# Performance work log

Hardware: AMD Instinct MI355X
Metric: run time of the kernel (lower is better)

## Reference

```python
import jax, jax.numpy as jnp
import numpy as np

B, S, E = 8, 1024, 1024
MS = 128            # modal_context seq len
NH = 16             # attention heads
NE = 8              # total experts (4 shared + 4 modality-specific)
TOP_K = 2
FF = 4 * E          # expert hidden dim
EPS = 1e-5


def layer_norm(x, w, b, eps=EPS):
    m = jnp.mean(x, axis=-1, keepdims=True)
    v = jnp.mean(jnp.square(x - m), axis=-1, keepdims=True)
    return (x - m) / jnp.sqrt(v + eps) * w + b


def mha(q_in, kv_in, in_w, in_b, out_w, out_b, nh=NH):
    # torch nn.MultiheadAttention (batch_first) equivalent, eval mode (no dropout)
    e = q_in.shape[-1]
    q = q_in @ in_w[:e].T + in_b[:e]
    k = kv_in @ in_w[e:2 * e].T + in_b[e:2 * e]
    v = kv_in @ in_w[2 * e:].T + in_b[2 * e:]
    b, sq, _ = q.shape
    sk = k.shape[1]
    hd = e // nh
    q = q.reshape(b, sq, nh, hd).transpose(0, 2, 1, 3)
    k = k.reshape(b, sk, nh, hd).transpose(0, 2, 1, 3)
    v = v.reshape(b, sk, nh, hd).transpose(0, 2, 1, 3)
    scores = jnp.einsum('bhqd,bhkd->bhqk', q, k) * (1.0 / np.sqrt(hd).astype(np.float32))
    attn = jax.nn.softmax(scores, axis=-1)
    o = jnp.einsum('bhqk,bhkd->bhqd', attn, v).transpose(0, 2, 1, 3).reshape(b, sq, e)
    return o @ out_w.T + out_b


def _forward(x, modal_context,
             attn_in_w, attn_in_b, attn_out_w, attn_out_b,
             xattn_in_w, xattn_in_b, xattn_out_w, xattn_out_b,
             norm1_w, norm1_b, norm2_w, norm2_b, norm3_w, norm3_b,
             xnorm_w, xnorm_b, router_w, router_b, gate_w, gate_b,
             exp_ln_w, exp_ln_b, exp_fc1_w, exp_fc1_b, exp_fc2_w, exp_fc2_b):
    # --- self-attention block (pre-norm residual) ---
    h = x + mha(layer_norm(x, norm1_w, norm1_b), layer_norm(x, norm1_w, norm1_b),
                attn_in_w, attn_in_b, attn_out_w, attn_out_b)
    # --- cross-modal fusion with sigmoid modal gate ---
    xn = layer_norm(h, xnorm_w, xnorm_b)
    fusion = mha(xn, modal_context, xattn_in_w, xattn_in_b, xattn_out_w, xattn_out_b)
    gate = jax.nn.sigmoid(xn @ gate_w.T + gate_b)
    h = h + gate * fusion
    # --- MoE block: AttentiveRouter (softmax + top-k renorm) over shared+modality experts ---
    xn2 = layer_norm(h, norm2_w, norm2_b)
    logits = xn2 @ router_w.T + router_b                  # [B,S,NE]
    probs = jax.nn.softmax(logits, axis=-1)
    topw, topi = jax.lax.top_k(probs, TOP_K)              # [B,S,K]
    topw = topw / jnp.sum(topw, axis=-1, keepdims=True)
    # scatter top-k weights to dense combine tensor [B,S,NE]
    combine = jnp.sum(jax.nn.one_hot(topi, NE, dtype=x.dtype) * topw[..., None], axis=-2)
    moe = jnp.zeros_like(h)
    for e_idx in range(NE):  # small fixed loop over experts
        xe = layer_norm(xn2, exp_ln_w[e_idx], exp_ln_b[e_idx])
        hh = jax.nn.gelu(xe @ exp_fc1_w[e_idx].T + exp_fc1_b[e_idx])
        oe = hh @ exp_fc2_w[e_idx].T + exp_fc2_b[e_idx]
        moe = moe + combine[..., e_idx:e_idx + 1] * oe
    out = h + moe
    return layer_norm(out, norm3_w, norm3_b)


def setup_inputs() -> dict:
    key = jax.random.key(0)
    ks = jax.random.split(key, 32)
    std = 0.02
    d = {
        'x': jax.random.normal(ks[0], (B, S, E), jnp.float32),
        'modal_context': jax.random.normal(ks[1], (B, MS, E), jnp.float32),
        'attn_in_w': jax.random.normal(ks[2], (3 * E, E), jnp.float32) * std,
        'attn_in_b': jnp.zeros((3 * E,), jnp.float32),
        'attn_out_w': jax.random.normal(ks[3], (E, E), jnp.float32) * std,
        'attn_out_b': jnp.zeros((E,), jnp.float32),
        'xattn_in_w': jax.random.normal(ks[4], (3 * E, E), jnp.float32) * std,
        'xattn_in_b': jnp.zeros((3 * E,), jnp.float32),
        'xattn_out_w': jax.random.normal(ks[5], (E, E), jnp.float32) * std,
        'xattn_out_b': jnp.zeros((E,), jnp.float32),
        'norm1_w': jnp.ones((E,), jnp.float32), 'norm1_b': jnp.zeros((E,), jnp.float32),
        'norm2_w': jnp.ones((E,), jnp.float32), 'norm2_b': jnp.zeros((E,), jnp.float32),
        'norm3_w': jnp.ones((E,), jnp.float32), 'norm3_b': jnp.zeros((E,), jnp.float32),
        'xnorm_w': jnp.ones((E,), jnp.float32), 'xnorm_b': jnp.zeros((E,), jnp.float32),
        'router_w': jax.random.normal(ks[6], (NE, E), jnp.float32) * 0.1 / np.sqrt(E).astype(np.float32),
        'router_b': jnp.zeros((NE,), jnp.float32),
        'gate_w': jax.random.normal(ks[7], (E, E), jnp.float32) * std,
        'gate_b': jnp.zeros((E,), jnp.float32),
        'exp_ln_w': jnp.ones((NE, E), jnp.float32),
        'exp_ln_b': jnp.zeros((NE, E), jnp.float32),
        'exp_fc1_w': jax.random.normal(ks[8], (NE, FF, E), jnp.float32) * std,
        'exp_fc1_b': jnp.zeros((NE, FF), jnp.float32),
        'exp_fc2_w': jax.random.normal(ks[9], (NE, E, FF), jnp.float32) * std,
        'exp_fc2_b': jnp.zeros((NE, E), jnp.float32),
    }
    return d


def reference(x, modal_context,
              attn_in_w, attn_in_b, attn_out_w, attn_out_b,
              xattn_in_w, xattn_in_b, xattn_out_w, xattn_out_b,
              norm1_w, norm1_b, norm2_w, norm2_b, norm3_w, norm3_b,
              xnorm_w, xnorm_b, router_w, router_b, gate_w, gate_b,
              exp_ln_w, exp_ln_b, exp_fc1_w, exp_fc1_b, exp_fc2_w, exp_fc2_b):
    return _forward(x, modal_context,
                    attn_in_w, attn_in_b, attn_out_w, attn_out_b,
                    xattn_in_w, xattn_in_b, xattn_out_w, xattn_out_b,
                    norm1_w, norm1_b, norm2_w, norm2_b, norm3_w, norm3_b,
                    xnorm_w, xnorm_b, router_w, router_b, gate_w, gate_b,
                    exp_ln_w, exp_ln_b, exp_fc1_w, exp_fc1_b, exp_fc2_w, exp_fc2_b)
```

## Files before the change

### kernel.cpp

```cpp
#include <hip/hip_runtime.h>
#include <cstdint>
#include <cstddef>
#include <math.h>

typedef unsigned short u16;
typedef __attribute__((ext_vector_type(4))) float f32x4;
typedef __attribute__((ext_vector_type(8))) short short8;
typedef __attribute__((ext_vector_type(4))) short short4v;

__device__ __forceinline__ float b2f(u16 u) {
    union { unsigned int i; float f; } v; v.i = ((unsigned int)u) << 16; return v.f;
}
__device__ __forceinline__ u16 f2b(float f) {
    union { float f; unsigned int i; } v; v.f = f;
    unsigned int i = v.i;
    return (u16)((i + 0x7FFFu + ((i >> 16) & 1u)) >> 16);
}
__device__ __forceinline__ void split3t(float a, short& h, short& m, short& l) {
    union { float f; unsigned int u; } va, vh, v1, vm, v2;
    va.f = a;
    vh.u = va.u & 0xFFFF0000u;
    float r1 = a - vh.f;
    v1.f = r1;
    vm.u = v1.u & 0xFFFF0000u;
    float r2 = r1 - vm.f;
    v2.f = r2;
    h = (short)(vh.u >> 16);
    m = (short)(vm.u >> 16);
    l = (short)(v2.u >> 16);
}
__device__ __forceinline__ float gelu_f(float x) {
    float x3 = x * x * x;
    float y = 0.7978845608028654f * (x + 0.044715f * x3);
    float ya = fminf(fabsf(y), 15.f);
    float e = expf(-2.f * ya);
    float t = (1.f - e) / (1.f + e);
    t = copysignf(t, y);
    return 0.5f * x * (1.f + t);
}
__device__ __forceinline__ void gld16(const u16* g, u16* l)
{
    __builtin_amdgcn_global_load_lds(
        (const __attribute__((address_space(1))) void*)(g),
        (__attribute__((address_space(3))) void*)(l),
        16, 0, 0);
}

struct EGemmP {
    const float* A; int lda; long aSo, aSi; int aDiv;
    const float* B; int ldb; long bSo, bSi; int bDiv;
    float* C; int ldc; long cSo, cSi; int cDiv;
    const float* bias;
    const float* resid;
    const float* fus;
    int K;
};

template<int EPI, int WM, int WN, int MF, int NF>
__global__ __launch_bounds__(256)
void gemm_emu(EGemmP p)
{
    constexpr int TM = WM * MF * 16;
    constexpr int TN = WN * NF * 16;
    constexpr int TK = 32;
    __shared__ u16 Ah[TM * TK], Am[TM * TK], Al[TM * TK];
    __shared__ u16 Bh[TN * TK], Bm[TN * TK], Bl[TN * TK];
    const int tid = threadIdx.x;
    const int z = blockIdx.z;
    const float* Ab = p.A + (long)(z / p.aDiv) * p.aSo + (long)(z % p.aDiv) * p.aSi
                      + (long)blockIdx.x * TM * p.lda;
    const float* Bb = p.B + (long)(z / p.bDiv) * p.bSo + (long)(z % p.bDiv) * p.bSi
                      + (long)blockIdx.y * TN * p.ldb;
    const int lane = tid & 63;
    const int wv = tid >> 6;
    const int wm = wv / WN;
    const int wn = wv % WN;
    const int kg = lane >> 4;
    const int l16 = lane & 15;
    f32x4 acc[MF][NF];
#pragma unroll
    for (int m = 0; m < MF; ++m)
#pragma unroll
        for (int n = 0; n < NF; ++n)
            acc[m][n] = (f32x4){0.f, 0.f, 0.f, 0.f};

    for (int k0 = 0; k0 < p.K; k0 += TK) {
#pragma unroll
        for (int i = 0; i < (TM * TK) / 1024; ++i) {
            int e = i * 256 + tid;
            int r = e >> 3;
            int c = (e & 7) * 4;
            f32x4 a = *(const f32x4*)&Ab[(long)r * p.lda + k0 + c];
            short4v h, m, l;
#pragma unroll
            for (int j = 0; j < 4; ++j) {
                short th, tm2, tl2;
                split3t(a[j], th, tm2, tl2);
                h[j] = th; m[j] = tm2; l[j] = tl2;
            }
            *(short4v*)&Ah[r * TK + c] = h;
            *(short4v*)&Am[r * TK + c] = m;
            *(short4v*)&Al[r * TK + c] = l;
        }
#pragma unroll
        for (int i = 0; i < (TN * TK) / 1024; ++i) {
            int e = i * 256 + tid;
            int r = e >> 3;
            int c = (e & 7) * 4;
            f32x4 a = *(const f32x4*)&Bb[(long)r * p.ldb + k0 + c];
            short4v h, m, l;
#pragma unroll
            for (int j = 0; j < 4; ++j) {
                short th, tm2, tl2;
                split3t(a[j], th, tm2, tl2);
                h[j] = th; m[j] = tm2; l[j] = tl2;
            }
            *(short4v*)&Bh[r * TK + c] = h;
            *(short4v*)&Bm[r * TK + c] = m;
            *(short4v*)&Bl[r * TK + c] = l;
        }
        __syncthreads();
        short8 ah[MF], am[MF], al[MF], bh[NF], bm[NF], bl[NF];
#pragma unroll
        for (int m = 0; m < MF; ++m) {
            int ro = (wm * MF * 16 + m * 16 + l16) * TK + kg * 8;
            ah[m] = *(const short8*)&Ah[ro];
            am[m] = *(const short8*)&Am[ro];
            al[m] = *(const short8*)&Al[ro];
        }
#pragma unroll
        for (int n = 0; n < NF; ++n) {
            int ro = (wn * NF * 16 + n * 16 + l16) * TK + kg * 8;
            bh[n] = *(const short8*)&Bh[ro];
            bm[n] = *(const short8*)&Bm[ro];
            bl[n] = *(const short8*)&Bl[ro];
        }
#pragma unroll
        for (int m = 0; m < MF; ++m)
#pragma unroll
            for (int n = 0; n < NF; ++n) {
                f32x4 a = acc[m][n];
                a = __builtin_amdgcn_mfma_f32_16x16x32_bf16(al[m], bh[n], a, 0, 0, 0);
                a = __builtin_amdgcn_mfma_f32_16x16x32_bf16(ah[m], bl[n], a, 0, 0, 0);
                a = __builtin_amdgcn_mfma_f32_16x16x32_bf16(am[m], bm[n], a, 0, 0, 0);
                a = __builtin_amdgcn_mfma_f32_16x16x32_bf16(am[m], bh[n], a, 0, 0, 0);
                a = __builtin_amdgcn_mfma_f32_16x16x32_bf16(ah[m], bm[n], a, 0, 0, 0);
                a = __builtin_amdgcn_mfma_f32_16x16x32_bf16(ah[m], bh[n], a, 0, 0, 0);
                acc[m][n] = a;
            }
        __syncthreads();
    }
    const long cbase = (long)(z / p.cDiv) * p.cSo + (long)(z % p.cDiv) * p.cSi;
#pragma unroll
    for (int m = 0; m < MF; ++m)
#pragma unroll
        for (int n = 0; n < NF; ++n) {
            const int colt = blockIdx.y * TN + wn * NF * 16 + n * 16 + l16;
            float bv = p.bias ? p.bias[colt] : 0.f;
#pragma unroll
            for (int r = 0; r < 4; ++r) {
                const int rowt = blockIdx.x * TM + wm * MF * 16 + m * 16 + kg * 4 + r;
                const long idx = cbase + (long)rowt * p.ldc + colt;
                float v = acc[m][n][r] + bv;
                if constexpr (EPI == 0) {
                    p.C[idx] = v;
                } else if constexpr (EPI == 1) {
                    p.C[idx] = v + p.resid[idx];
                } else {
                    float g = 1.f / (1.f + expf(-v));
                    p.C[idx] = p.resid[idx] + g * p.fus[idx];
                }
            }
        }
}

struct MoeP {
    const u16* A; int lda;
    const u16* Bw; long bStrideE; int ldb;
    u16* HHo;
    float* M1; float* M2;
    int ldc;
    const float* biasE; long biasStride;
    const float* combine;
    const int* cnt;
    const int* pfx;
    const int* tlist;
    int K;
};

template<int EPI>
__global__ __launch_bounds__(256)
void gemm_moe(MoeP p)
{
    const int ex = blockIdx.z;
    const int count = p.cnt[ex];
    if ((int)(blockIdx.x * 128) >= count) return;
    const int base = p.pfx[ex];
    constexpr int TK = 64;
    __shared__ __align__(16) u16 lA[128 * TK];
    __shared__ __align__(16) u16 lB[128 * TK];
    const int tid = threadIdx.x;
    const u16* Ab = p.A + (long)(base + blockIdx.x * 128) * p.lda;
    const u16* Bb = p.Bw + (long)ex * p.bStrideE + (long)blockIdx.y * 128 * p.ldb;
    const int lane = tid & 63;
    const int wv = tid >> 6;
    const int wm = wv >> 1;
    const int wn = wv & 1;
    const int kg = lane >> 4;
    const int l16 = lane & 15;
    f32x4 acc[4][4];
#pragma unroll
    for (int m = 0; m < 4; ++m)
#pragma unroll
        for (int n = 0; n < 4; ++n)
            acc[m][n] = (f32x4){0.f, 0.f, 0.f, 0.f};

    const u16* pa[4]; const u16* pb[4]; u16* la[4]; u16* lb[4];
#pragma unroll
    for (int i = 0; i < 4; ++i) {
        int e = i * 256 + tid;
        int r = e >> 3;
        int jg = (e & 7) ^ (r & 7);
        pa[i] = &Ab[(long)r * p.lda + jg * 8];
        pb[i] = &Bb[(long)r * p.ldb + jg * 8];
        la[i] = &lA[e * 8];
        lb[i] = &lB[e * 8];
    }

    for (int k0 = 0; k0 < p.K; k0 += TK) {
#pragma unroll
        for (int i = 0; i < 4; ++i) {
            gld16(pa[i] + k0, la[i]);
            gld16(pb[i] + k0, lb[i]);
        }
        __syncthreads();
#pragma unroll
        for (int ks = 0; ks < 2; ++ks) {
            short8 af[4], bfr[4];
#pragma unroll
            for (int m = 0; m < 4; ++m) {
                int row = wm * 64 + m * 16 + l16;
                int jj = (ks * 4 + kg) ^ (row & 7);
                af[m] = *(const short8*)&lA[row * TK + jj * 8];
            }
#pragma unroll
            for (int n = 0; n < 4; ++n) {
                int row = wn * 64 + n * 16 + l16;
                int jj = (ks * 4 + kg) ^ (row & 7);
                bfr[n] = *(const short8*)&lB[row * TK + jj * 8];
            }
#pragma unroll
            for (int m = 0; m < 4; ++m)
#pragma unroll
                for (int n = 0; n < 4; ++n)
                    acc[m][n] = __builtin_amdgcn_mfma_f32_16x16x32_bf16(af[m], bfr[n], acc[m][n], 0, 0, 0);
        }
        __syncthreads();
    }
    const float* bias = p.biasE + (long)ex * p.biasStride;
#pragma unroll
    for (int m = 0; m < 4; ++m)
#pragma unroll
        for (int n = 0; n < 4; ++n) {
            const int colt = blockIdx.y * 128 + wn * 64 + n * 16 + l16;
            const float bv = bias[colt];
#pragma unroll
            for (int r = 0; r < 4; ++r) {
                const int rowt = blockIdx.x * 128 + wm * 64 + m * 16 + kg * 4 + r;
                if (rowt >= count) continue;
                float v = acc[m][n][r] + bv;
                if constexpr (EPI == 3) {
                    p.HHo[(long)(base + rowt) * p.ldc + colt] = f2b(gelu_f(v));
                } else {
                    const int entry = p.tlist[ex * 8192 + rowt];
                    const int tok = entry & 0xFFFF;
                    const int k = entry >> 16;
                    const float w = p.combine[(long)tok * 8 + ex];
                    float* dst = k ? p.M2 : p.M1;
                    dst[(long)tok * p.ldc + colt] = w * v;
                }
            }
        }
}

template<int MODE>
__global__ __launch_bounds__(256)
void ln2p(const float* in, const float* add1, const float* add2,
          const float* w, const float* b, float* outf)
{
    const long row = blockIdx.x;
    const int t = threadIdx.x;
    const int c0 = t * 4;
    f32x4 v = *(const f32x4*)&in[row * 1024 + c0];
    if constexpr (MODE == 2) {
        f32x4 a1 = *(const f32x4*)&add1[row * 1024 + c0];
        f32x4 a2 = *(const f32x4*)&add2[row * 1024 + c0];
#pragma unroll
        for (int j = 0; j < 4; ++j) v[j] += a1[j] + a2[j];
    }
    __shared__ float r1[4], r2[4];
    const int lane = t & 63, wv = t >> 6;
    float s1 = v[0] + v[1] + v[2] + v[3];
    for (int o = 32; o; o >>= 1) s1 += __shfl_xor(s1, o);
    if (lane == 0) r1[wv] = s1;
    __syncthreads();
    const float mean = (r1[0] + r1[1] + r1[2] + r1[3]) * (1.f / 1024.f);
    f32x4 d;
#pragma unroll
    for (int j = 0; j < 4; ++j) d[j] = v[j] - mean;
    float s2 = d[0] * d[0] + d[1] * d[1] + d[2] * d[2] + d[3] * d[3];
    for (int o = 32; o; o >>= 1) s2 += __shfl_xor(s2, o);
    if (lane == 0) r2[wv] = s2;
    __syncthreads();
    const float var = (r2[0] + r2[1] + r2[2] + r2[3]) * (1.f / 1024.f);
    const float rstd = 1.f / sqrtf(var + 1e-5f);
    f32x4 o4;
#pragma unroll
    for (int j = 0; j < 4; ++j) o4[j] = d[j] * rstd * w[c0 + j] + b[c0 + j];
    *(f32x4*)&outf[row * 1024 + c0] = o4;
}

__global__ __launch_bounds__(256)
void rowstats(const float* in, float* st, int* cnt)
{
    if (blockIdx.x == 0 && threadIdx.x < 8) cnt[threadIdx.x] = 0;
    const long row = blockIdx.x;
    const int t = threadIdx.x;
    const int c0 = t * 4;
    f32x4 v = *(const f32x4*)&in[row * 1024 + c0];
    __shared__ float r1[4], r2[4];
    const int lane = t & 63, wv = t >> 6;
    float s1 = v[0] + v[1] + v[2] + v[3];
    for (int o = 32; o; o >>= 1) s1 += __shfl_xor(s1, o);
    if (lane == 0) r1[wv] = s1;
    __syncthreads();
    const float mean = (r1[0] + r1[1] + r1[2] + r1[3]) * (1.f / 1024.f);
    float s2 = 0.f;
#pragma unroll
    for (int j = 0; j < 4; ++j) { float d = v[j] - mean; s2 += d * d; }
    for (int o = 32; o; o >>= 1) s2 += __shfl_xor(s2, o);
    if (lane == 0) r2[wv] = s2;
    __syncthreads();
    if (t == 0) {
        const float var = (r2[0] + r2[1] + r2[2] + r2[3]) * (1.f / 1024.f);
        st[row * 2] = mean;
        st[row * 2 + 1] = 1.f / sqrtf(var + 1e-5f);
    }
}

__global__ __launch_bounds__(256)
void softmax_f32(float* sm, int C, float scale)
{
    const long row = blockIdx.x;
    float* p = sm + row * (long)C;
    const int t = threadIdx.x;
    const int idx = t * 4;
    const bool act = idx < C;
    f32x4 v = (f32x4){-1e30f, -1e30f, -1e30f, -1e30f};
    if (act) {
        v = *(const f32x4*)&p[idx];
#pragma unroll
        for (int j = 0; j < 4; ++j) v[j] *= scale;
    }
    float mx = fmaxf(fmaxf(v[0], v[1]), fmaxf(v[2], v[3]));
    for (int o = 32; o; o >>= 1) mx = fmaxf(mx, __shfl_xor(mx, o));
    __shared__ float red[4], red2[4];
    const int lane = t & 63, wv = t >> 6;
    if (lane == 0) red[wv] = mx;
    __syncthreads();
    mx = fmaxf(fmaxf(red[0], red[1]), fmaxf(red[2], red[3]));
    float e[4], s = 0.f;
    if (act) {
#pragma unroll
        for (int j = 0; j < 4; ++j) { e[j] = expf(v[j] - mx); s += e[j]; }
    }
    for (int o = 32; o; o >>= 1) s += __shfl_xor(s, o);
    if (lane == 0) red2[wv] = s;
    __syncthreads();
    s = red2[0] + red2[1] + red2[2] + red2[3];
    if (act) {
        f32x4 o4;
#pragma unroll
        for (int j = 0; j < 4; ++j) o4[j] = e[j] / s;
        *(f32x4*)&p[idx] = o4;
    }
}

__global__ __launch_bounds__(256)
void transpose64f(const float* src, int sld, long sSo, long sSi, int sDiv, float* dst, int Skv)
{
    const int z = blockIdx.y;
    const float* Sp = src + (long)(z / sDiv) * sSo + (long)(z % sDiv) * sSi;
    float* Dp = dst + (long)z * 64 * Skv;
    const int j0 = blockIdx.x * 64;
    __shared__ float tl[64][68];
    const int tid = threadIdx.x;
#pragma unroll
    for (int it = 0; it < 4; ++it) {
        int e = (it * 256 + tid) * 4;
        int r = e >> 6, c = e & 63;
        f32x4 d = *(const f32x4*)&Sp[(long)(j0 + r) * sld + c];
        *(f32x4*)&tl[r][c] = d;
    }
    __syncthreads();
    const int d0 = tid >> 2;
    const int jc = (tid & 3) * 16;
    float tmp[16];
#pragma unroll
    for (int i = 0; i < 16; ++i) tmp[i] = tl[jc + i][d0];
#pragma unroll
    for (int i = 0; i < 16; ++i) Dp[(long)d0 * Skv + j0 + jc + i] = tmp[i];
}

__global__ __launch_bounds__(256)
void router_k(const float* xn2, const float* rw, const float* rb, float* cmb,
              int* cnt, int* tlist)
{
    const int tok = blockIdx.x * 4 + (threadIdx.x >> 6);
    const int lane = threadIdx.x & 63;
    const float* xp = xn2 + (long)tok * 1024 + lane * 16;
    float xv[16];
#pragma unroll
    for (int j = 0; j < 16; ++j) xv[j] = xp[j];
    double acc[8];
#pragma unroll
    for (int e = 0; e < 8; ++e) {
        const float* wp = rw + e * 1024 + lane * 16;
        double s = 0.0;
#pragma unroll
        for (int j = 0; j < 16; ++j) s += (double)xv[j] * (double)wp[j];
        acc[e] = s;
    }
    for (int o = 32; o; o >>= 1) {
#pragma unroll
        for (int e = 0; e < 8; ++e) acc[e] += __shfl_xor(acc[e], o);
    }
    if (lane == 0) {
        double l[8];
#pragma unroll
        for (int e = 0; e < 8; ++e) l[e] = acc[e] + (double)rb[e];
        int i1 = 0;
#pragma unroll
        for (int e = 1; e < 8; ++e) if (l[e] > l[i1]) i1 = e;
        int i2 = (i1 == 0) ? 1 : 0;
#pragma unroll
        for (int e = 0; e < 8; ++e) if (e != i1 && l[e] > l[i2]) i2 = e;
        double w1 = 1.0 / (1.0 + exp(l[i2] - l[i1]));
        double w2 = 1.0 - w1;
        float c8[8] = {0, 0, 0, 0, 0, 0, 0, 0};
        c8[i1] = (float)w1;
        c8[i2] = (float)w2;
        float* cp = cmb + (long)tok * 8;
#pragma unroll
        for (int e = 0; e < 8; ++e) cp[e] = c8[e];
        int s1 = atomicAdd(&cnt[i1], 1);
        tlist[i1 * 8192 + s1] = tok;
        int s2 = atomicAdd(&cnt[i2], 1);
        tlist[i2 * 8192 + s2] = tok | 65536;
    }
}

__global__ void prefix8(const int* cnt, int* pfx)
{
    if (threadIdx.x == 0) {
        int s = 0;
#pragma unroll
        for (int e = 0; e < 8; ++e) { pfx[e] = s; s += cnt[e]; }
    }
}

__global__ __launch_bounds__(256)
void gather_all(const float* xn2, const float* st, const int* cnt, const int* pfx,
                const int* tlist, const float* lnw, const float* lnb, u16* xe)
{
    const int e = blockIdx.y;
    const int slot = blockIdx.x;
    if (slot >= cnt[e]) return;
    const int tok = tlist[e * 8192 + slot] & 0xFFFF;
    const int c0 = threadIdx.x * 4;
    f32x4 v = *(const f32x4*)&xn2[(long)tok * 1024 + c0];
    const float m = st[tok * 2], r = st[tok * 2 + 1];
    const float* w = lnw + (long)e * 1024;
    const float* b = lnb + (long)e * 1024;
    short4v o4;
#pragma unroll
    for (int j = 0; j < 4; ++j) o4[j] = (short)f2b((v[j] - m) * r * w[c0 + j] + b[c0 + j]);
    *(short4v*)&xe[(long)(pfx[e] + slot) * 1024 + c0] = o4;
}

__global__ __launch_bounds__(256)
void cvtw(const float* in, u16* out, long n4)
{
    const long stride = (long)gridDim.x * 256;
    for (long i = (long)blockIdx.x * 256 + threadIdx.x; i < n4; i += stride) {
        f32x4 v = *(const f32x4*)&in[i * 4];
        short4v o;
#pragma unroll
        for (int j = 0; j < 4; ++j) o[j] = (short)f2b(v[j]);
        *(short4v*)&out[i * 4] = o;
    }
}

extern "C" void kernel_launch(void* const* d_in, const int* in_sizes, int n_in,
                              void* d_out, int out_size, void* d_ws, size_t ws_size,
                              hipStream_t stream)
{
    (void)in_sizes; (void)n_in; (void)out_size;
    const float* x          = (const float*)d_in[0];
    const float* modal      = (const float*)d_in[1];
    const float* attn_in_w  = (const float*)d_in[2];
    const float* attn_in_b  = (const float*)d_in[3];
    const float* attn_out_w = (const float*)d_in[4];
    const float* attn_out_b = (const float*)d_in[5];
    const float* xattn_in_w = (const float*)d_in[6];
    const float* xattn_in_b = (const float*)d_in[7];
    const float* xattn_out_w= (const float*)d_in[8];
    const float* xattn_out_b= (const float*)d_in[9];
    const float* norm1_w = (const float*)d_in[10];
    const float* norm1_b = (const float*)d_in[11];
    const float* norm2_w = (const float*)d_in[12];
    const float* norm2_b = (const float*)d_in[13];
    const float* norm3_w = (const float*)d_in[14];
    const float* norm3_b = (const float*)d_in[15];
    const float* xnorm_w = (const float*)d_in[16];
    const float* xnorm_b = (const float*)d_in[17];
    const float* router_w = (const float*)d_in[18];
    const float* router_b = (const float*)d_in[19];
    const float* gate_w = (const float*)d_in[20];
    const float* gate_b = (const float*)d_in[21];
    const float* exp_ln_w = (const float*)d_in[22];
    const float* exp_ln_b = (const float*)d_in[23];
    const float* exp_fc1_w = (const float*)d_in[24];
    const float* exp_fc1_b = (const float*)d_in[25];
    const float* exp_fc2_w = (const float*)d_in[26];
    const float* exp_fc2_b = (const float*)d_in[27];

    char* wsb = (char*)d_ws;
    size_t off = 0;
    auto AL = [&](size_t bytes) { size_t r = off; off += (bytes + 255) & ~(size_t)255; return r; };
    float* XN  = (float*)(wsb + AL(33554432));
    float* H   = (float*)(wsb + AL(33554432));
    float* H2  = (float*)(wsb + AL(33554432));
    float* XN2 = (float*)(wsb + AL(33554432));
    float* FUS = (float*)(wsb + AL(33554432));
    float* MOE = (float*)(wsb + AL(33554432));
    float* XKV = (float*)(wsb + AL(8388608));
    float* CMB = (float*)(wsb + AL(262144));
    float* ST  = (float*)(wsb + AL(65536));
    int*   CNT = (int*)(wsb + AL(256));
    int*   PFX = (int*)(wsb + AL(256));
    int*   TLS = (int*)(wsb + AL(262144));
    char*  RA  = wsb + AL(100663296);
    char*  RB  = wsb + AL(100663296);
    if (off > ws_size) return;

    float* QKV = (float*)RA;
    float* XQ  = (float*)RA;
    float* XO  = (float*)(RA + 33554432);
    float* SCf = (float*)RB;
    float* VTf = (float*)(RB + 67108864);
    float* SC2 = H2;
    u16*   HH  = (u16*)RA;
    u16*   XE  = (u16*)(RA + 135266304);
    u16*   WB  = (u16*)XN;
    float* out = (float*)d_out;

    ln2p<0><<<8192, 256, 0, stream>>>(x, nullptr, nullptr, norm1_w, norm1_b, XN);

    {
        EGemmP p{XN, 1024, 0, 0, 1, attn_in_w, 1024, 0, 0, 1,
                 QKV, 3072, 0, 0, 1, attn_in_b, nullptr, nullptr, 1024};
        gemm_emu<0, 2, 2, 4, 2><<<dim3(64, 48, 1), 256, 0, stream>>>(p);
    }
    transpose64f<<<dim3(16, 128), 256, 0, stream>>>(QKV + 2048, 3072, (long)1024 * 3072, 64, 16, VTf, 1024);

    for (int g = 0; g < 4; ++g) {
        EGemmP s{QKV + (long)g * 2 * 1024 * 3072, 3072, (long)1024 * 3072, 64, 16,
                 QKV + 1024 + (long)g * 2 * 1024 * 3072, 3072, (long)1024 * 3072, 64, 16,
                 SC2, 1024, 0, (long)1024 * 1024, 1 << 20, nullptr, nullptr, nullptr, 64};
        gemm_emu<0, 2, 2, 4, 2><<<dim3(8, 16, 32), 256, 0, stream>>>(s);

        softmax_f32<<<32 * 1024, 256, 0, stream>>>(SC2, 1024, 0.125f);

        EGemmP v{SC2, 1024, 0, (long)1024 * 1024, 1 << 20,
                 VTf + (long)g * 32 * 64 * 1024, 1024, 0, (long)64 * 1024, 1 << 20,
                 XN + (long)g * 2 * 1024 * 1024, 1024, (long)1024 * 1024, 64, 16,
                 nullptr, nullptr, nullptr, 1024};
        gemm_emu<0, 2, 2, 2, 2><<<dim3(16, 1, 32), 256, 0, stream>>>(v);
    }

    {
        EGemmP p{XN, 1024, 0, 0, 1, attn_out_w, 1024, 0, 0, 1,
                 H, 1024, 0, 0, 1, attn_out_b, x, nullptr, 1024};
        gemm_emu<1, 2, 2, 4, 2><<<dim3(64, 16, 1), 256, 0, stream>>>(p);
    }
    ln2p<0><<<8192, 256, 0, stream>>>(H, nullptr, nullptr, xnorm_w, xnorm_b, XN);

    {
        EGemmP p{XN, 1024, 0, 0, 1, xattn_in_w, 1024, 0, 0, 1,
                 XQ, 1024, 0, 0, 1, xattn_in_b, nullptr, nullptr, 1024};
        gemm_emu<0, 2, 2, 4, 2><<<dim3(64, 16, 1), 256, 0, stream>>>(p);
    }
    {
        EGemmP p{modal, 1024, 0, 0, 1, xattn_in_w + (size_t)1024 * 1024, 1024, 0, 0, 1,
                 XKV, 2048, 0, 0, 1, xattn_in_b + 1024, nullptr, nullptr, 1024};
        gemm_emu<0, 2, 2, 4, 2><<<dim3(8, 32, 1), 256, 0, stream>>>(p);
    }
    transpose64f<<<dim3(2, 128), 256, 0, stream>>>(XKV + 1024, 2048, (long)128 * 2048, 64, 16, VTf, 128);

    {
        EGemmP s{XQ, 1024, (long)1024 * 1024, 64, 16,
                 XKV, 2048, (long)128 * 2048, 64, 16,
                 SCf, 128, 0, (long)1024 * 128, 1 << 20, nullptr, nullptr, nullptr, 64};
        gemm_emu<0, 2, 2, 4, 2><<<dim3(8, 2, 128), 256, 0, stream>>>(s);
    }
    softmax_f32<<<128 * 1024, 256, 0, stream>>>(SCf, 128, 0.125f);
    {
        EGemmP v{SCf, 128, 0, (long)1024 * 128, 1 << 20,
                 VTf, 128, 0, (long)64 * 128, 1 << 20,
                 XO, 1024, (long)1024 * 1024, 64, 16, nullptr, nullptr, nullptr, 128};
        gemm_emu<0, 2, 2, 4, 2><<<dim3(8, 1, 128), 256, 0, stream>>>(v);
    }
    {
        EGemmP p{XO, 1024, 0, 0, 1, xattn_out_w, 1024, 0, 0, 1,
                 FUS, 1024, 0, 0, 1, xattn_out_b, nullptr, nullptr, 1024};
        gemm_emu<0, 2, 2, 4, 2><<<dim3(64, 16, 1), 256, 0, stream>>>(p);
    }
    {
        EGemmP p{XN, 1024, 0, 0, 1, gate_w, 1024, 0, 0, 1,
                 H2, 1024, 0, 0, 1, gate_b, H, FUS, 1024};
        gemm_emu<2, 2, 2, 4, 2><<<dim3(64, 16, 1), 256, 0, stream>>>(p);
    }
    ln2p<0><<<8192, 256, 0, stream>>>(H2, nullptr, nullptr, norm2_w, norm2_b, XN2);
    rowstats<<<8192, 256, 0, stream>>>(XN2, ST, CNT);
    router_k<<<2048, 256, 0, stream>>>(XN2, router_w, router_b, CMB, CNT, TLS);
    prefix8<<<1, 64, 0, stream>>>(CNT, PFX);

    gather_all<<<dim3(8192, 8), 256, 0, stream>>>(XN2, ST, CNT, PFX, TLS, exp_ln_w, exp_ln_b, XE);
    cvtw<<<2048, 256, 0, stream>>>(exp_fc1_w, WB, 8388608);
    {
        MoeP p1{XE, 1024, WB, (long)4096 * 1024, 1024,
                HH, nullptr, nullptr, 4096,
                exp_fc1_b, 4096, nullptr, CNT, PFX, TLS, 1024};
        gemm_moe<3><<<dim3(64, 32, 8), 256, 0, stream>>>(p1);
    }
    cvtw<<<2048, 256, 0, stream>>>(exp_fc2_w, WB, 8388608);
    {
        MoeP p2{HH, 4096, WB, (long)1024 * 4096, 4096,
                nullptr, MOE, FUS, 1024,
                exp_fc2_b, 1024, CMB, CNT, PFX, TLS, 4096};
        gemm_moe<4><<<dim3(64, 8, 8), 256, 0, stream>>>(p2);
    }

    ln2p<2><<<8192, 256, 0, stream>>>(H2, MOE, FUS, norm3_w, norm3_b, out);
}
```

Before: 2.780 ms.

## Split-K the attention PV GEMM and narrow fc2 MoE tiles for more blocks

The P·V attention GEMM, which previously launched only 16x32 blocks with K=1024, is now split into four K-chunks of 256 (128 z-slices). Partial results go to a scratch buffer and a new pvred kernel sums them and scatters into the head-interleaved output. The MoE GEMM gains an NF template parameter so the fc2 pass uses 64-wide N tiles, doubling its grid to raise occupancy. The cost is extra partial-sum memory traffic, an extra kernel launch per group, and lower per-block reuse of the A tile in fc2.

```diff
diff --git a/kernel.cpp b/kernel.cpp
--- a/kernel.cpp
+++ b/kernel.cpp
@@ -188,55 +188,63 @@
     int K;
 };
 
-template<int EPI>
+template<int EPI, int NF>
 __global__ __launch_bounds__(256)
 void gemm_moe(MoeP p)
 {
+    constexpr int TN = 2 * NF * 16;
+    constexpr int TK = 64;
+    constexpr int BCH = TN / 32;
     const int ex = blockIdx.z;
     const int count = p.cnt[ex];
     if ((int)(blockIdx.x * 128) >= count) return;
     const int base = p.pfx[ex];
-    constexpr int TK = 64;
     __shared__ __align__(16) u16 lA[128 * TK];
-    __shared__ __align__(16) u16 lB[128 * TK];
+    __shared__ __align__(16) u16 lB[TN * TK];
     const int tid = threadIdx.x;
     const u16* Ab = p.A + (long)(base + blockIdx.x * 128) * p.lda;
-    const u16* Bb = p.Bw + (long)ex * p.bStrideE + (long)blockIdx.y * 128 * p.ldb;
+    const u16* Bb = p.Bw + (long)ex * p.bStrideE + (long)blockIdx.y * TN * p.ldb;
     const int lane = tid & 63;
     const int wv = tid >> 6;
     const int wm = wv >> 1;
     const int wn = wv & 1;
     const int kg = lane >> 4;
     const int l16 = lane & 15;
-    f32x4 acc[4][4];
+    f32x4 acc[4][NF];
 #pragma unroll
     for (int m = 0; m < 4; ++m)
 #pragma unroll
-        for (int n = 0; n < 4; ++n)
+        for (int n = 0; n < NF; ++n)
             acc[m][n] = (f32x4){0.f, 0.f, 0.f, 0.f};
 
-    const u16* pa[4]; const u16* pb[4]; u16* la[4]; u16* lb[4];
+    const u16* pa[4]; u16* la[4];
 #pragma unroll
     for (int i = 0; i < 4; ++i) {
         int e = i * 256 + tid;
         int r = e >> 3;
         int jg = (e & 7) ^ (r & 7);
         pa[i] = &Ab[(long)r * p.lda + jg * 8];
+        la[i] = &lA[e * 8];
+    }
+    const u16* pb[BCH]; u16* lb[BCH];
+#pragma unroll
+    for (int i = 0; i < BCH; ++i) {
+        int e = i * 256 + tid;
+        int r = e >> 3;
+        int jg = (e & 7) ^ (r & 7);
         pb[i] = &Bb[(long)r * p.ldb + jg * 8];
-        la[i] = &lA[e * 8];
         lb[i] = &lB[e * 8];
     }
 
     for (int k0 = 0; k0 < p.K; k0 += TK) {
 #pragma unroll
-        for (int i = 0; i < 4; ++i) {
-            gld16(pa[i] + k0, la[i]);
-            gld16(pb[i] + k0, lb[i]);
-        }
+        for (int i = 0; i < 4; ++i) gld16(pa[i] + k0, la[i]);
+#pragma unroll
+        for (int i = 0; i < BCH; ++i) gld16(pb[i] + k0, lb[i]);
         __syncthreads();
 #pragma unroll
         for (int ks = 0; ks < 2; ++ks) {
-            short8 af[4], bfr[4];
+            short8 af[4], bfr[NF];
 #pragma unroll
             for (int m = 0; m < 4; ++m) {
                 int row = wm * 64 + m * 16 + l16;
@@ -244,15 +252,15 @@
                 af[m] = *(const short8*)&lA[row * TK + jj * 8];
             }
 #pragma unroll
-            for (int n = 0; n < 4; ++n) {
-                int row = wn * 64 + n * 16 + l16;
+            for (int n = 0; n < NF; ++n) {
+                int row = wn * NF * 16 + n * 16 + l16;
                 int jj = (ks * 4 + kg) ^ (row & 7);
                 bfr[n] = *(const short8*)&lB[row * TK + jj * 8];
             }
 #pragma unroll
             for (int m = 0; m < 4; ++m)
 #pragma unroll
-                for (int n = 0; n < 4; ++n)
+                for (int n = 0; n < NF; ++n)
                     acc[m][n] = __builtin_amdgcn_mfma_f32_16x16x32_bf16(af[m], bfr[n], acc[m][n], 0, 0, 0);
         }
         __syncthreads();
@@ -261,8 +269,8 @@
 #pragma unroll
     for (int m = 0; m < 4; ++m)
 #pragma unroll
-        for (int n = 0; n < 4; ++n) {
-            const int colt = blockIdx.y * 128 + wn * 64 + n * 16 + l16;
+        for (int n = 0; n < NF; ++n) {
+            const int colt = blockIdx.y * TN + wn * NF * 16 + n * 16 + l16;
             const float bv = bias[colt];
 #pragma unroll
             for (int r = 0; r < 4; ++r) {
@@ -410,6 +418,27 @@
     for (int i = 0; i < 16; ++i) tmp[i] = tl[jc + i][d0];
 #pragma unroll
     for (int i = 0; i < 16; ++i) Dp[(long)d0 * Skv + j0 + jc + i] = tmp[i];
+}
+
+__global__ __launch_bounds__(256)
+void pvred(const float* pp, float* xn, int g)
+{
+    const long i = (long)blockIdx.x * 256 + threadIdx.x;
+    const long e = i * 4;
+    const int z = (int)(e >> 16);
+    const int rem = (int)(e & 65535);
+    const int row = rem >> 6;
+    const int col = rem & 63;
+    f32x4 a = *(const f32x4*)&pp[e];
+    f32x4 b = *(const f32x4*)&pp[2097152 + e];
+    f32x4 c = *(const f32x4*)&pp[2 * 2097152 + e];
+    f32x4 d = *(const f32x4*)&pp[3 * 2097152 + e];
+    f32x4 s;
+#pragma unroll
+    for (int j = 0; j < 4; ++j) s[j] = (a[j] + b[j]) + (c[j] + d[j]);
+    float* dst = xn + (long)g * 2097152 + (long)(z >> 4) * 1048576
+               + (long)row * 1024 + (z & 15) * 64 + col;
+    *(f32x4*)dst = s;
 }
 
 __global__ __launch_bounds__(256)
@@ -558,6 +587,7 @@
     float* XQ  = (float*)RA;
     float* XO  = (float*)(RA + 33554432);
     float* SCf = (float*)RB;
+    float* PP  = (float*)RB;
     float* VTf = (float*)(RB + 67108864);
     float* SC2 = H2;
     u16*   HH  = (u16*)RA;
@@ -582,11 +612,12 @@
 
         softmax_f32<<<32 * 1024, 256, 0, stream>>>(SC2, 1024, 0.125f);
 
-        EGemmP v{SC2, 1024, 0, (long)1024 * 1024, 1 << 20,
-                 VTf + (long)g * 32 * 64 * 1024, 1024, 0, (long)64 * 1024, 1 << 20,
-                 XN + (long)g * 2 * 1024 * 1024, 1024, (long)1024 * 1024, 64, 16,
-                 nullptr, nullptr, nullptr, 1024};
-        gemm_emu<0, 2, 2, 2, 2><<<dim3(16, 1, 32), 256, 0, stream>>>(v);
+        EGemmP v{SC2, 1024, 256, (long)1024 * 1024, 32,
+                 VTf + (long)g * 32 * 64 * 1024, 1024, 256, (long)64 * 1024, 32,
+                 PP, 64, 2097152, 65536, 32, nullptr, nullptr, nullptr, 256};
+        gemm_emu<0, 2, 2, 2, 2><<<dim3(16, 1, 128), 256, 0, stream>>>(v);
+
+        pvred<<<2048, 256, 0, stream>>>(PP, XN, g);
     }
 
     {
@@ -642,14 +673,14 @@
         MoeP p1{XE, 1024, WB, (long)4096 * 1024, 1024,
                 HH, nullptr, nullptr, 4096,
                 exp_fc1_b, 4096, nullptr, CNT, PFX, TLS, 1024};
-        gemm_moe<3><<<dim3(64, 32, 8), 256, 0, stream>>>(p1);
+        gemm_moe<3, 4><<<dim3(64, 32, 8), 256, 0, stream>>>(p1);
     }
     cvtw<<<2048, 256, 0, stream>>>(exp_fc2_w, WB, 8388608);
     {
         MoeP p2{HH, 4096, WB, (long)1024 * 4096, 4096,
                 nullptr, MOE, FUS, 1024,
                 exp_fc2_b, 1024, CMB, CNT, PFX, TLS, 4096};
-        gemm_moe<4><<<dim3(64, 8, 8), 256, 0, stream>>>(p2);
+        gemm_moe<4, 2><<<dim3(64, 16, 8), 256, 0, stream>>>(p2);
     }
 
     ln2p<2><<<8192, 256, 0, stream>>>(H2, MOE, FUS, norm3_w, norm3_b, out);
```

New measurement: 2.782 ms. About the same (+0.1%).
